# Performance work log

Measured on AMD Instinct MI355X. Metric: run time of the kernel, lower is better.

The kernel has to match this reference:

```python
import jax, jax.numpy as jnp
import numpy as np

D_MODEL = 1024
N_HEADS = 16
HEAD_DIM = D_MODEL // N_HEADS
SEQ_LEN = 2048
D_FF = 4 * D_MODEL
LCC_SCALE = 0.1
LN_EPS = 1e-5
NORM_EPS = 1e-12  # F.normalize eps


def _layer_norm(x, g, b):
    mu = jnp.mean(x, axis=-1, keepdims=True)
    var = jnp.mean(jnp.square(x - mu), axis=-1, keepdims=True)
    return (x - mu) * jax.lax.rsqrt(var + LN_EPS) * g + b


def setup_inputs() -> dict:
    key = jax.random.key(0)
    ks = jax.random.split(key, 8)
    s = 0.02  # weight init scale
    return {
        "x": jax.random.normal(ks[0], (SEQ_LEN, D_MODEL), jnp.float32),
        "lcc_values": jax.random.uniform(ks[1], (SEQ_LEN,), jnp.float32),
        "w_qkv": jax.random.normal(ks[2], (D_MODEL, 3 * D_MODEL), jnp.float32) * s,
        "b_qkv": jnp.zeros((3 * D_MODEL,), jnp.float32),
        "w_out": jax.random.normal(ks[3], (D_MODEL, D_MODEL), jnp.float32) * s,
        "b_out": jnp.zeros((D_MODEL,), jnp.float32),
        "ln1_g": jnp.ones((D_MODEL,), jnp.float32),
        "ln1_b": jnp.zeros((D_MODEL,), jnp.float32),
        "ln2_g": jnp.ones((D_MODEL,), jnp.float32),
        "ln2_b": jnp.zeros((D_MODEL,), jnp.float32),
        "w_ff1": jax.random.normal(ks[4], (D_MODEL, D_FF), jnp.float32) * s,
        "b_ff1": jnp.zeros((D_FF,), jnp.float32),
        "w_ff2": jax.random.normal(ks[5], (D_FF, D_MODEL), jnp.float32) * s,
        "b_ff2": jnp.zeros((D_MODEL,), jnp.float32),
    }


def reference(x, lcc_values, w_qkv, b_qkv, w_out, b_out, ln1_g, ln1_b,
              ln2_g, ln2_b, w_ff1, b_ff1, w_ff2, b_ff2):
    L = x.shape[0]
    scaling = HEAD_DIM ** -0.5

    normed = _layer_norm(x, ln1_g, ln1_b)
    qkv = normed @ w_qkv + b_qkv                      # [L, 3D]
    qkv = qkv.reshape(L, 3, N_HEADS, HEAD_DIM)
    q = jnp.transpose(qkv[:, 0], (1, 0, 2))           # [H, L, d]
    k = jnp.transpose(qkv[:, 1], (1, 0, 2))
    v = jnp.transpose(qkv[:, 2], (1, 0, 2))

    # cosine attention: L2-normalize q, k
    q = q / jnp.maximum(jnp.linalg.norm(q, axis=-1, keepdims=True), NORM_EPS)
    k = k / jnp.maximum(jnp.linalg.norm(k, axis=-1, keepdims=True), NORM_EPS)
    q = q * scaling

    scores = jnp.einsum('hld,hmd->hlm', q, k)         # [H, L, L]
    bias = (lcc_values[:, None] + lcc_values[None, :]) * 0.5 * LCC_SCALE
    scores = jnp.clip(scores + bias[None], -10.0, 10.0)
    probs = jax.nn.softmax(scores, axis=-1)

    attn = jnp.einsum('hlm,hmd->hld', probs, v)       # [H, L, d]
    attn = jnp.transpose(attn, (1, 0, 2)).reshape(L, D_MODEL)
    x = x + (attn @ w_out + b_out)

    normed2 = _layer_norm(x, ln2_g, ln2_b)
    h = jax.nn.gelu(normed2 @ w_ff1 + b_ff1, approximate=False)
    x = x + (h @ w_ff2 + b_ff2)
    return x
```

## Files before the change

kernel.cpp:

```cpp
#include <hip/hip_runtime.h>
#include <hip/hip_bf16.h>

#define D_MODEL 1024
#define SEQ 2048
#define NH 16
#define HD 64
#define DFF 4096

typedef __attribute__((ext_vector_type(8))) __bf16 bf16x8;
typedef __attribute__((ext_vector_type(4))) float f32x4;

__device__ __forceinline__ unsigned short f2bf(float f) {
    union { float f; unsigned u; } v; v.f = f;
    unsigned r = v.u + 0x7fffu + ((v.u >> 16) & 1u);
    return (unsigned short)(r >> 16);
}
__device__ __forceinline__ unsigned pack2(float a, float b) {
    return (unsigned)f2bf(a) | ((unsigned)f2bf(b) << 16);
}
__device__ __forceinline__ float bf2f(unsigned short u) {
    union { unsigned u; float f; } v; v.u = ((unsigned)u) << 16;
    return v.f;
}
__device__ __forceinline__ bf16x8 ld_frag(const unsigned short* p) {
    union { uint4 u; bf16x8 b; } c;
    c.u = *(const uint4*)p;
    return c.b;
}
__device__ __forceinline__ void load16(const float* p, float* v) {
#pragma unroll
    for (int i = 0; i < 4; i++) {
        float4 f = ((const float4*)p)[i];
        v[4*i+0]=f.x; v[4*i+1]=f.y; v[4*i+2]=f.z; v[4*i+3]=f.w;
    }
}

typedef __attribute__((address_space(3))) unsigned lds_u32;
typedef const __attribute__((address_space(1))) unsigned glob_u32;
__device__ __forceinline__ void gl_lds16(const unsigned short* g, unsigned short* l) {
    __builtin_amdgcn_global_load_lds((glob_u32*)g, (lds_u32*)l, 16, 0, 0);
}

#define MFMA16(a,b,c) __builtin_amdgcn_mfma_f32_16x16x32_bf16(a,b,c,0,0,0)

__global__ __launch_bounds__(256) void wcast_t(const float* __restrict__ W,
                                               unsigned short* __restrict__ Wt,
                                               int K, int N) {
    __shared__ unsigned short lt[64][72];
    int t = threadIdx.x;
    int nb = blockIdx.x, kb = blockIdx.y;
    int r = t >> 2, c0 = (t & 3) << 4;
    const float* src = W + (size_t)(kb*64 + r) * N + nb*64 + c0;
    float4 f0 = ((const float4*)src)[0];
    float4 f1 = ((const float4*)src)[1];
    float4 f2 = ((const float4*)src)[2];
    float4 f3 = ((const float4*)src)[3];
    unsigned* dst = (unsigned*)&lt[r][c0];
    dst[0]=pack2(f0.x,f0.y); dst[1]=pack2(f0.z,f0.w);
    dst[2]=pack2(f1.x,f1.y); dst[3]=pack2(f1.z,f1.w);
    dst[4]=pack2(f2.x,f2.y); dst[5]=pack2(f2.z,f2.w);
    dst[6]=pack2(f3.x,f3.y); dst[7]=pack2(f3.z,f3.w);
    __syncthreads();
    int n_ = t >> 2, k0 = (t & 3) << 4;
    unsigned obuf[8];
#pragma unroll
    for (int i = 0; i < 8; i++)
        obuf[i] = (unsigned)lt[k0 + 2*i][n_] | ((unsigned)lt[k0 + 2*i + 1][n_] << 16);
    unsigned short* out = Wt + (size_t)(nb*64 + n_) * K + kb*64 + k0;
    ((uint4*)out)[0] = *(uint4*)&obuf[0];
    ((uint4*)out)[1] = *(uint4*)&obuf[4];
}

__global__ __launch_bounds__(256) void ln_kernel(const float* __restrict__ x,
                                                 const float* __restrict__ g,
                                                 const float* __restrict__ b,
                                                 unsigned short* __restrict__ out) {
    int row = blockIdx.x, t = threadIdx.x;
    float4 v = ((const float4*)(x + (size_t)row * D_MODEL))[t];
    float s  = v.x + v.y + v.z + v.w;
    float sq = v.x*v.x + v.y*v.y + v.z*v.z + v.w*v.w;
#pragma unroll
    for (int m = 1; m < 64; m <<= 1) { s += __shfl_xor(s, m, 64); sq += __shfl_xor(sq, m, 64); }
    __shared__ float ls[4], lq[4];
    int wave = t >> 6, lane = t & 63;
    if (lane == 0) { ls[wave] = s; lq[wave] = sq; }
    __syncthreads();
    s  = ls[0]+ls[1]+ls[2]+ls[3];
    sq = lq[0]+lq[1]+lq[2]+lq[3];
    float mu  = s * (1.0f / D_MODEL);
    float var = sq * (1.0f / D_MODEL) - mu * mu;
    float rs  = rsqrtf(var + 1e-5f);
    int c = t * 4;
    float y0 = (v.x - mu) * rs * g[c+0] + b[c+0];
    float y1 = (v.y - mu) * rs * g[c+1] + b[c+1];
    float y2 = (v.z - mu) * rs * g[c+2] + b[c+2];
    float y3 = (v.w - mu) * rs * g[c+3] + b[c+3];
    unsigned* o = (unsigned*)(out + (size_t)row * D_MODEL + c);
    o[0] = pack2(y0, y1); o[1] = pack2(y2, y3);
}

template<int NP>
__global__ __launch_bounds__(256) void reduce_k(const float* __restrict__ res,
                                                const float* __restrict__ bias,
                                                const unsigned short* __restrict__ parts,
                                                float* __restrict__ out,
                                                int MN, int Ndiv4) {
    int i = blockIdx.x * 256 + threadIdx.x;
    float4 r = ((const float4*)res)[i];
    float4 b = ((const float4*)bias)[i & (Ndiv4 - 1)];
    r.x += b.x; r.y += b.y; r.z += b.z; r.w += b.w;
#pragma unroll
    for (int p = 0; p < NP; p++) {
        ushort4 u = ((const ushort4*)(parts + (size_t)p * MN))[i];
        r.x += bf2f(u.x); r.y += bf2f(u.y); r.z += bf2f(u.z); r.w += bf2f(u.w);
    }
    ((float4*)out)[i] = r;
}

template<int TM, int TN, int SPLITK, int GELU, int RES, int OUTBF, int PART>
__global__ __launch_bounds__(256) void gemm_bt(const unsigned short* __restrict__ A,
                                               const unsigned short* __restrict__ Bt,
                                               const float* __restrict__ bias,
                                               const float* __restrict__ res,
                                               void* __restrict__ C,
                                               int M, int N, int K) {
    constexpr int ISS = TM / 32;
    constexpr int MI = TM / 32;
    constexpr int NI = TN / 32;
    __shared__ unsigned short lA[TM * 64];
    __shared__ unsigned short lB[TN * 64];
    int t = threadIdx.x;
    int bn = blockIdx.x, bm = blockIdx.y;
    int kz = (SPLITK > 1) ? blockIdx.z : 0;
    int KS = K / SPLITK;
    int K0 = kz * KS;
    int wave = t >> 6, lane = t & 63;
    int quad = lane >> 4, lr = lane & 15;

    const unsigned short* pa[ISS];
    unsigned short* la[ISS];
#pragma unroll
    for (int i = 0; i < ISS; i++) {
        int rl = wave*(TM/4) + i*8 + (lane >> 3);
        int ss = (lane & 7) ^ (rl & 7);
        pa[i] = A + (size_t)(bm*TM + rl) * K + K0 + ss*8;
        la[i] = lA + (wave*(TM/4) + i*8) * 64;
    }
    const unsigned short* pb[ISS];
    unsigned short* lb[ISS];
#pragma unroll
    for (int i = 0; i < ISS; i++) {
        int rl = wave*(TN/4) + i*8 + (lane >> 3);
        int ss = (lane & 7) ^ (rl & 7);
        pb[i] = Bt + (size_t)(bn*TN + rl) * K + K0 + ss*8;
        lb[i] = lB + (wave*(TN/4) + i*8) * 64;
    }

    int wr = (wave >> 1) * (TM/2), wc = (wave & 1) * (TN/2);
    const unsigned short* fa[2][MI];
#pragma unroll
    for (int i = 0; i < MI; i++) {
        int row = wr + i*16 + lr;
        fa[0][i] = lA + row*64 + ((quad     ^ (row & 7)))*8;
        fa[1][i] = lA + row*64 + (((quad+4) ^ (row & 7)))*8;
    }
    const unsigned short* fb[2][NI];
#pragma unroll
    for (int j = 0; j < NI; j++) {
        int row = wc + j*16 + lr;
        fb[0][j] = lB + row*64 + ((quad     ^ (row & 7)))*8;
        fb[1][j] = lB + row*64 + (((quad+4) ^ (row & 7)))*8;
    }

    f32x4 z = {0.f, 0.f, 0.f, 0.f};
    f32x4 acc[MI][NI];
#pragma unroll
    for (int i = 0; i < MI; i++)
#pragma unroll
        for (int j = 0; j < NI; j++) acc[i][j] = z;

    for (int kk = 0; kk < KS; kk += 64) {
#pragma unroll
        for (int i = 0; i < ISS; i++) gl_lds16(pa[i] + kk, la[i]);
#pragma unroll
        for (int i = 0; i < ISS; i++) gl_lds16(pb[i] + kk, lb[i]);
        __syncthreads();
#pragma unroll
        for (int h = 0; h < 2; h++) {
            bf16x8 af[MI], bfr[NI];
#pragma unroll
            for (int i = 0; i < MI; i++) af[i]  = ld_frag(fa[h][i]);
#pragma unroll
            for (int j = 0; j < NI; j++) bfr[j] = ld_frag(fb[h][j]);
#pragma unroll
            for (int i = 0; i < MI; i++)
#pragma unroll
                for (int j = 0; j < NI; j++)
                    acc[i][j] = MFMA16(af[i], bfr[j], acc[i][j]);
        }
        __syncthreads();
    }

    if (PART) {
        unsigned short* P = (unsigned short*)C + (size_t)kz * M * N;
#pragma unroll
        for (int i = 0; i < MI; i++)
#pragma unroll
            for (int j = 0; j < NI; j++) {
                int row0 = bm*TM + wr + i*16 + quad*4;
                int col  = bn*TN + wc + j*16 + lr;
#pragma unroll
                for (int r = 0; r < 4; r++)
                    P[(size_t)(row0 + r) * N + col] = f2bf(acc[i][j][r]);
            }
    } else {
#pragma unroll
        for (int i = 0; i < MI; i++)
#pragma unroll
            for (int j = 0; j < NI; j++) {
                int row0 = bm*TM + wr + i*16 + quad*4;
                int col  = bn*TN + wc + j*16 + lr;
                float bv = bias[col];
#pragma unroll
                for (int r = 0; r < 4; r++) {
                    float v = acc[i][j][r] + bv;
                    if (RES)  v += res[(size_t)(row0 + r) * N + col];
                    if (GELU) v = 0.5f * v * (1.0f + erff(v * 0.70710678118654752f));
                    if (OUTBF) ((unsigned short*)C)[(size_t)(row0 + r) * N + col] = f2bf(v);
                    else       ((float*)C)[(size_t)(row0 + r) * N + col] = v;
                }
            }
    }
}

__global__ __launch_bounds__(256) void qkv_post(const float* __restrict__ qkv,
                                                unsigned short* __restrict__ qn,
                                                unsigned short* __restrict__ kn,
                                                unsigned short* __restrict__ vt) {
    __shared__ unsigned short lv[64][72];
    int h = blockIdx.x, lb = blockIdx.y;
    int t = threadIdx.x;
    int lloc = t >> 2, seg = (t & 3) << 4;
    int lg = lb*64 + lloc;
    const float* row = qkv + (size_t)lg * 3072;
    float vq[16], vk[16], vv[16];
    load16(row + h*64 + seg, vq);
    load16(row + 1024 + h*64 + seg, vk);
    load16(row + 2048 + h*64 + seg, vv);
    float sq = 0.f, sk = 0.f;
#pragma unroll
    for (int i = 0; i < 16; i++) { sq += vq[i]*vq[i]; sk += vk[i]*vk[i]; }
    sq += __shfl_xor(sq, 1, 64); sq += __shfl_xor(sq, 2, 64);
    sk += __shfl_xor(sk, 1, 64); sk += __shfl_xor(sk, 2, 64);
    float scq = 0.125f / fmaxf(sqrtf(sq), 1e-12f);
    float sck = 1.0f   / fmaxf(sqrtf(sk), 1e-12f);
    unsigned* oq = (unsigned*)(qn + ((size_t)h*SEQ + lg)*HD + seg);
    unsigned* ok = (unsigned*)(kn + ((size_t)h*SEQ + lg)*HD + seg);
#pragma unroll
    for (int i = 0; i < 8; i++) {
        oq[i] = pack2(vq[2*i]*scq, vq[2*i+1]*scq);
        ok[i] = pack2(vk[2*i]*sck, vk[2*i+1]*sck);
    }
    unsigned* lvp = (unsigned*)&lv[lloc][seg];
#pragma unroll
    for (int i = 0; i < 8; i++) lvp[i] = pack2(vv[2*i], vv[2*i+1]);
    __syncthreads();
    int dloc = t >> 2, l0 = (t & 3) << 4;
    unsigned obuf[8];
#pragma unroll
    for (int i = 0; i < 8; i++)
        obuf[i] = (unsigned)lv[l0 + 2*i][dloc] | ((unsigned)lv[l0 + 2*i + 1][dloc] << 16);
    unsigned short* ov = vt + ((size_t)h*HD + dloc)*SEQ + lb*64 + l0;
    ((uint4*)ov)[0] = *(uint4*)&obuf[0];
    ((uint4*)ov)[1] = *(uint4*)&obuf[4];
}

__global__ __launch_bounds__(256) void attn_kernel(const unsigned short* __restrict__ qn,
                                                   const unsigned short* __restrict__ kn,
                                                   const unsigned short* __restrict__ vt,
                                                   const float* __restrict__ lcc,
                                                   unsigned short* __restrict__ attn) {
    __shared__ unsigned short lQ[64][72];
    __shared__ unsigned short lK[64][72];
    __shared__ unsigned short lV[64][72];
    __shared__ unsigned short lP[64][72];
    __shared__ float lL[SEQ];
    int h = blockIdx.x, qb = blockIdx.y;
    int t = threadIdx.x;
    int rl = t >> 2, c0 = (t & 3) << 4;
    const unsigned short* pq = qn + ((size_t)h*SEQ + qb*64 + rl)*HD + c0;
    *(uint4*)&lQ[rl][c0]     = ((const uint4*)pq)[0];
    *(uint4*)&lQ[rl][c0 + 8] = ((const uint4*)pq)[1];
    for (int i = t; i < SEQ; i += 256) lL[i] = 0.05f * lcc[i];
    __syncthreads();
    int wave = t >> 6, lane = t & 63, quad = lane >> 4, lr = lane & 15;
    float lqv[4];
#pragma unroll
    for (int r = 0; r < 4; r++) lqv[r] = lL[qb*64 + wave*16 + quad*4 + r];
    bf16x8 aq0 = ld_frag(&lQ[wave*16 + lr][quad*8]);
    bf16x8 aq1 = ld_frag(&lQ[wave*16 + lr][32 + quad*8]);
    f32x4 z = {0.f, 0.f, 0.f, 0.f};
    f32x4 oacc[4]; oacc[0]=z; oacc[1]=z; oacc[2]=z; oacc[3]=z;
    float den[4] = {0.f, 0.f, 0.f, 0.f};

    for (int kb = 0; kb < SEQ/64; kb++) {
        __syncthreads();
        const unsigned short* pk = kn + ((size_t)h*SEQ + kb*64 + rl)*HD + c0;
        uint4 k0v = ((const uint4*)pk)[0], k1v = ((const uint4*)pk)[1];
        const unsigned short* pv = vt + ((size_t)h*HD + rl)*SEQ + kb*64 + c0;
        uint4 v0v = ((const uint4*)pv)[0], v1v = ((const uint4*)pv)[1];
        *(uint4*)&lK[rl][c0]     = k0v; *(uint4*)&lK[rl][c0 + 8] = k1v;
        *(uint4*)&lV[rl][c0]     = v0v; *(uint4*)&lV[rl][c0 + 8] = v1v;
        __syncthreads();
#pragma unroll
        for (int j = 0; j < 4; j++) {
            bf16x8 b0 = ld_frag(&lK[j*16 + lr][quad*8]);
            bf16x8 b1 = ld_frag(&lK[j*16 + lr][32 + quad*8]);
            f32x4 s = z;
            s = MFMA16(aq0, b0, s);
            s = MFMA16(aq1, b1, s);
            float lm = lL[kb*64 + j*16 + lr];
#pragma unroll
            for (int r = 0; r < 4; r++) {
                float sv = s[r] + lqv[r] + lm;
                sv = fminf(fmaxf(sv, -10.f), 10.f);
                float p = __expf(sv);
                den[r] += p;
                lP[wave*16 + quad*4 + r][j*16 + lr] = f2bf(p);
            }
        }
        bf16x8 ap0 = ld_frag(&lP[wave*16 + lr][quad*8]);
        bf16x8 ap1 = ld_frag(&lP[wave*16 + lr][32 + quad*8]);
#pragma unroll
        for (int j2 = 0; j2 < 4; j2++) {
            bf16x8 b0 = ld_frag(&lV[j2*16 + lr][quad*8]);
            bf16x8 b1 = ld_frag(&lV[j2*16 + lr][32 + quad*8]);
            oacc[j2] = MFMA16(ap0, b0, oacc[j2]);
            oacc[j2] = MFMA16(ap1, b1, oacc[j2]);
        }
    }
#pragma unroll
    for (int r = 0; r < 4; r++)
#pragma unroll
        for (int m = 1; m < 16; m <<= 1) den[r] += __shfl_xor(den[r], m, 64);
#pragma unroll
    for (int j2 = 0; j2 < 4; j2++)
#pragma unroll
        for (int r = 0; r < 4; r++) {
            float ov = oacc[j2][r] / den[r];
            int rowg = qb*64 + wave*16 + quad*4 + r;
            int colg = h*64 + j2*16 + lr;
            attn[(size_t)rowg * D_MODEL + colg] = f2bf(ov);
        }
}

extern "C" void kernel_launch(void* const* d_in, const int* in_sizes, int n_in,
                              void* d_out, int out_size, void* d_ws, size_t ws_size,
                              hipStream_t stream) {
    const float* x      = (const float*)d_in[0];
    const float* lcc    = (const float*)d_in[1];
    const float* w_qkv  = (const float*)d_in[2];
    const float* b_qkv  = (const float*)d_in[3];
    const float* w_out  = (const float*)d_in[4];
    const float* b_out  = (const float*)d_in[5];
    const float* ln1_g  = (const float*)d_in[6];
    const float* ln1_b  = (const float*)d_in[7];
    const float* ln2_g  = (const float*)d_in[8];
    const float* ln2_b  = (const float*)d_in[9];
    const float* w_ff1  = (const float*)d_in[10];
    const float* b_ff1  = (const float*)d_in[11];
    const float* w_ff2  = (const float*)d_in[12];
    const float* b_ff2  = (const float*)d_in[13];

    char* ws = (char*)d_ws;
    unsigned short* wtq  = (unsigned short*)(ws);
    unsigned short* wto  = (unsigned short*)(ws + 6291456);
    unsigned short* wtf1 = (unsigned short*)(ws + 8388608);
    unsigned short* wtf2 = (unsigned short*)(ws + 16777216);
    unsigned short* xn   = (unsigned short*)(ws + 25165824);
    float*          qkvb = (float*)(ws + 29360128);
    float*          x1   = (float*)(ws + 29360128);
    unsigned short* hbuf = (unsigned short*)(ws + 37748736);
    unsigned short* pOP  = (unsigned short*)(ws + 37748736);
    unsigned short* qnb  = (unsigned short*)(ws + 54525952);
    unsigned short* knb  = (unsigned short*)(ws + 58720256);
    unsigned short* vtb  = (unsigned short*)(ws + 62914560);
    unsigned short* pFF2 = (unsigned short*)(ws);
    unsigned short* attnb = xn;
    unsigned short* x2n  = qnb;
    float* outp = (float*)d_out;

    wcast_t<<<dim3(48, 16), 256, 0, stream>>>(w_qkv, wtq, 1024, 3072);
    wcast_t<<<dim3(16, 16), 256, 0, stream>>>(w_out, wto, 1024, 1024);
    wcast_t<<<dim3(64, 16), 256, 0, stream>>>(w_ff1, wtf1, 1024, 4096);
    wcast_t<<<dim3(16, 64), 256, 0, stream>>>(w_ff2, wtf2, 4096, 1024);
    ln_kernel<<<SEQ, 256, 0, stream>>>(x, ln1_g, ln1_b, xn);
    gemm_bt<128,128,1,0,0,0,0><<<dim3(24, 16), 256, 0, stream>>>(xn, wtq, b_qkv, nullptr, qkvb, SEQ, 3072, 1024);
    qkv_post<<<dim3(16, 32), 256, 0, stream>>>(qkvb, qnb, knb, vtb);
    attn_kernel<<<dim3(16, 32), 256, 0, stream>>>(qnb, knb, vtb, lcc, attnb);
    gemm_bt<128,128,2,0,0,0,1><<<dim3(8, 16, 2), 256, 0, stream>>>(attnb, wto, nullptr, nullptr, pOP, SEQ, 1024, 1024);
    reduce_k<2><<<SEQ*D_MODEL/1024, 256, 0, stream>>>(x, b_out, pOP, x1, SEQ*D_MODEL, D_MODEL/4);
    ln_kernel<<<SEQ, 256, 0, stream>>>(x1, ln2_g, ln2_b, x2n);
    gemm_bt<128,128,1,1,0,1,0><<<dim3(32, 16), 256, 0, stream>>>(x2n, wtf1, b_ff1, nullptr, hbuf, SEQ, 4096, 1024);
    gemm_bt<128,128,4,0,0,0,1><<<dim3(8, 16, 4), 256, 0, stream>>>(hbuf, wtf2, nullptr, nullptr, pFF2, SEQ, 1024, 4096);
    reduce_k<4><<<SEQ*D_MODEL/1024, 256, 0, stream>>>(x1, b_ff2, pFF2, outp, SEQ*D_MODEL, D_MODEL/4);
}
```

Baseline: 291.8 us.

## Register-prefetch GEMM and attention tiles, fold log2e into exp2, drop clip

The GEMM stops using direct global-to-LDS loads and instead prefetches the next K tile into registers while the current tile runs on MFMA. The attention kernel gets the same register prefetch for its K/V tiles. It also folds log2e into the q scale and the LCC bias so it can use exp2, seeds the MFMA accumulator with the bias, and drops the clip, which cannot trigger because cosine scores are bounded. LDS row padding shrinks from 72 to 68, which leaves 16-byte fragment reads misaligned and may split them or add bank conflicts.

Measured after the change: 576.5 us. 1.98x slower.

```diff
diff --git a/kernel.cpp b/kernel.cpp
--- a/kernel.cpp
+++ b/kernel.cpp
@@ -35,13 +35,8 @@
     }
 }
 
-typedef __attribute__((address_space(3))) unsigned lds_u32;
-typedef const __attribute__((address_space(1))) unsigned glob_u32;
-__device__ __forceinline__ void gl_lds16(const unsigned short* g, unsigned short* l) {
-    __builtin_amdgcn_global_load_lds((glob_u32*)g, (lds_u32*)l, 16, 0, 0);
-}
-
 #define MFMA16(a,b,c) __builtin_amdgcn_mfma_f32_16x16x32_bf16(a,b,c,0,0,0)
+#define LOG2E 1.4426950408889634f
 
 __global__ __launch_bounds__(256) void wcast_t(const float* __restrict__ W,
                                                unsigned short* __restrict__ Wt,
@@ -144,7 +139,7 @@
         int rl = wave*(TM/4) + i*8 + (lane >> 3);
         int ss = (lane & 7) ^ (rl & 7);
         pa[i] = A + (size_t)(bm*TM + rl) * K + K0 + ss*8;
-        la[i] = lA + (wave*(TM/4) + i*8) * 64;
+        la[i] = lA + (wave*(TM/4) + i*8) * 64 + lane*8;
     }
     const unsigned short* pb[ISS];
     unsigned short* lb[ISS];
@@ -153,7 +148,7 @@
         int rl = wave*(TN/4) + i*8 + (lane >> 3);
         int ss = (lane & 7) ^ (rl & 7);
         pb[i] = Bt + (size_t)(bn*TN + rl) * K + K0 + ss*8;
-        lb[i] = lB + (wave*(TN/4) + i*8) * 64;
+        lb[i] = lB + (wave*(TN/4) + i*8) * 64 + lane*8;
     }
 
     int wr = (wave >> 1) * (TM/2), wc = (wave & 1) * (TN/2);
@@ -179,12 +174,22 @@
 #pragma unroll
         for (int j = 0; j < NI; j++) acc[i][j] = z;
 
+    uint4 ra[ISS], rb[ISS];
+#pragma unroll
+    for (int i = 0; i < ISS; i++) { ra[i] = *(const uint4*)(pa[i]); rb[i] = *(const uint4*)(pb[i]); }
+
     for (int kk = 0; kk < KS; kk += 64) {
-#pragma unroll
-        for (int i = 0; i < ISS; i++) gl_lds16(pa[i] + kk, la[i]);
-#pragma unroll
-        for (int i = 0; i < ISS; i++) gl_lds16(pb[i] + kk, lb[i]);
         __syncthreads();
+#pragma unroll
+        for (int i = 0; i < ISS; i++) { *(uint4*)la[i] = ra[i]; *(uint4*)lb[i] = rb[i]; }
+        __syncthreads();
+        if (kk + 64 < KS) {
+#pragma unroll
+            for (int i = 0; i < ISS; i++) {
+                ra[i] = *(const uint4*)(pa[i] + kk + 64);
+                rb[i] = *(const uint4*)(pb[i] + kk + 64);
+            }
+        }
 #pragma unroll
         for (int h = 0; h < 2; h++) {
             bf16x8 af[MI], bfr[NI];
@@ -198,7 +203,6 @@
                 for (int j = 0; j < NI; j++)
                     acc[i][j] = MFMA16(af[i], bfr[j], acc[i][j]);
         }
-        __syncthreads();
     }
 
     if (PART) {
@@ -252,8 +256,8 @@
     for (int i = 0; i < 16; i++) { sq += vq[i]*vq[i]; sk += vk[i]*vk[i]; }
     sq += __shfl_xor(sq, 1, 64); sq += __shfl_xor(sq, 2, 64);
     sk += __shfl_xor(sk, 1, 64); sk += __shfl_xor(sk, 2, 64);
-    float scq = 0.125f / fmaxf(sqrtf(sq), 1e-12f);
-    float sck = 1.0f   / fmaxf(sqrtf(sk), 1e-12f);
+    float scq = (0.125f * LOG2E) / fmaxf(sqrtf(sq), 1e-12f);
+    float sck = 1.0f / fmaxf(sqrtf(sk), 1e-12f);
     unsigned* oq = (unsigned*)(qn + ((size_t)h*SEQ + lg)*HD + seg);
     unsigned* ok = (unsigned*)(kn + ((size_t)h*SEQ + lg)*HD + seg);
 #pragma unroll
@@ -280,10 +284,10 @@
                                                    const unsigned short* __restrict__ vt,
                                                    const float* __restrict__ lcc,
                                                    unsigned short* __restrict__ attn) {
-    __shared__ unsigned short lQ[64][72];
-    __shared__ unsigned short lK[64][72];
-    __shared__ unsigned short lV[64][72];
-    __shared__ unsigned short lP[64][72];
+    __shared__ unsigned short lQ[64][68];
+    __shared__ unsigned short lK[64][68];
+    __shared__ unsigned short lV[64][68];
+    __shared__ unsigned short lP[64][68];
     __shared__ float lL[SEQ];
     int h = blockIdx.x, qb = blockIdx.y;
     int t = threadIdx.x;
@@ -291,40 +295,45 @@
     const unsigned short* pq = qn + ((size_t)h*SEQ + qb*64 + rl)*HD + c0;
     *(uint4*)&lQ[rl][c0]     = ((const uint4*)pq)[0];
     *(uint4*)&lQ[rl][c0 + 8] = ((const uint4*)pq)[1];
-    for (int i = t; i < SEQ; i += 256) lL[i] = 0.05f * lcc[i];
+    for (int i = t; i < SEQ; i += 256) lL[i] = (0.05f * LOG2E) * lcc[i];
     __syncthreads();
     int wave = t >> 6, lane = t & 63, quad = lane >> 4, lr = lane & 15;
-    float lqv[4];
-#pragma unroll
-    for (int r = 0; r < 4; r++) lqv[r] = lL[qb*64 + wave*16 + quad*4 + r];
+    float biasq[4];
+#pragma unroll
+    for (int r = 0; r < 4; r++) biasq[r] = lL[qb*64 + wave*16 + quad*4 + r];
     bf16x8 aq0 = ld_frag(&lQ[wave*16 + lr][quad*8]);
     bf16x8 aq1 = ld_frag(&lQ[wave*16 + lr][32 + quad*8]);
     f32x4 z = {0.f, 0.f, 0.f, 0.f};
     f32x4 oacc[4]; oacc[0]=z; oacc[1]=z; oacc[2]=z; oacc[3]=z;
     float den[4] = {0.f, 0.f, 0.f, 0.f};
 
+    const unsigned short* pk0 = kn + (size_t)h*SEQ*HD + rl*HD + c0;
+    const unsigned short* pv0 = vt + ((size_t)h*HD + rl)*SEQ + c0;
+    uint4 k0v = ((const uint4*)pk0)[0], k1v = ((const uint4*)pk0)[1];
+    uint4 v0v = ((const uint4*)pv0)[0], v1v = ((const uint4*)pv0)[1];
+
     for (int kb = 0; kb < SEQ/64; kb++) {
         __syncthreads();
-        const unsigned short* pk = kn + ((size_t)h*SEQ + kb*64 + rl)*HD + c0;
-        uint4 k0v = ((const uint4*)pk)[0], k1v = ((const uint4*)pk)[1];
-        const unsigned short* pv = vt + ((size_t)h*HD + rl)*SEQ + kb*64 + c0;
-        uint4 v0v = ((const uint4*)pv)[0], v1v = ((const uint4*)pv)[1];
         *(uint4*)&lK[rl][c0]     = k0v; *(uint4*)&lK[rl][c0 + 8] = k1v;
         *(uint4*)&lV[rl][c0]     = v0v; *(uint4*)&lV[rl][c0 + 8] = v1v;
         __syncthreads();
+        if (kb + 1 < SEQ/64) {
+            const unsigned short* pk = pk0 + (size_t)(kb+1)*64*HD;
+            const unsigned short* pv = pv0 + (kb+1)*64;
+            k0v = ((const uint4*)pk)[0]; k1v = ((const uint4*)pk)[1];
+            v0v = ((const uint4*)pv)[0]; v1v = ((const uint4*)pv)[1];
+        }
 #pragma unroll
         for (int j = 0; j < 4; j++) {
             bf16x8 b0 = ld_frag(&lK[j*16 + lr][quad*8]);
             bf16x8 b1 = ld_frag(&lK[j*16 + lr][32 + quad*8]);
-            f32x4 s = z;
+            float lm = lL[kb*64 + j*16 + lr];
+            f32x4 s = {biasq[0] + lm, biasq[1] + lm, biasq[2] + lm, biasq[3] + lm};
             s = MFMA16(aq0, b0, s);
             s = MFMA16(aq1, b1, s);
-            float lm = lL[kb*64 + j*16 + lr];
 #pragma unroll
             for (int r = 0; r < 4; r++) {
-                float sv = s[r] + lqv[r] + lm;
-                sv = fminf(fmaxf(sv, -10.f), 10.f);
-                float p = __expf(sv);
+                float p = exp2f(s[r]);
                 den[r] += p;
                 lP[wave*16 + quad*4 + r][j*16 + lr] = f2bf(p);
             }
@@ -343,11 +352,14 @@
     for (int r = 0; r < 4; r++)
 #pragma unroll
         for (int m = 1; m < 16; m <<= 1) den[r] += __shfl_xor(den[r], m, 64);
+    float inv[4];
+#pragma unroll
+    for (int r = 0; r < 4; r++) inv[r] = 1.0f / den[r];
 #pragma unroll
     for (int j2 = 0; j2 < 4; j2++)
 #pragma unroll
         for (int r = 0; r < 4; r++) {
-            float ov = oacc[j2][r] / den[r];
+            float ov = oacc[j2][r] * inv[r];
             int rowg = qb*64 + wave*16 + quad*4 + r;
             int colg = h*64 + j2*16 + lr;
             attn[(size_t)rowg * D_MODEL + colg] = f2bf(ov);
```
